# Kernel tuning notes

Measured on AMD Instinct MI355X. Metric: run time of the kernel, lower is better.

## Reference

```python
import jax, jax.numpy as jnp
import numpy as np

N_NODES = 50000
N_EDGES = 800000
IN_CH = 256
OUT_CH = 64
HEADS = 4


def setup_inputs() -> dict:
    key = jax.random.key(0)
    k1, k2, k3, k4, k5 = jax.random.split(key, 5)
    x = jax.random.normal(k1, (N_NODES, IN_CH), dtype=jnp.float32)
    edge_index = jax.random.randint(k2, (2, N_EDGES), 0, N_NODES, dtype=jnp.int64)
    # xavier-ish scaled params
    weight = jax.random.normal(k3, (HEADS, IN_CH, OUT_CH), dtype=jnp.float32) * (2.0 / (IN_CH + OUT_CH)) ** 0.5
    att_src = jax.random.normal(k4, (1, HEADS, OUT_CH), dtype=jnp.float32) * 0.1
    att_dst = jax.random.normal(k5, (1, HEADS, OUT_CH), dtype=jnp.float32) * 0.1
    bias = jnp.zeros((HEADS * OUT_CH,), dtype=jnp.float32)
    return {"x": x, "edge_index": edge_index, "weight": weight,
            "att_src": att_src, "att_dst": att_dst, "bias": bias}


def reference(x, edge_index, weight, att_src, att_dst, bias):
    # GATConv forward (eval mode: dropout is identity), vectorized over heads.
    num_nodes = x.shape[0]
    row, col = edge_index[0], edge_index[1]
    # per-head projection: [N, H, C]
    x_h = jnp.einsum('nf,hfc->nhc', x, weight)
    alpha_src = jnp.sum(x_h * att_src[0], axis=-1)   # [N, H]
    alpha_dst = jnp.sum(x_h * att_dst[0], axis=-1)   # [N, H]
    alpha = alpha_src[row] + alpha_dst[col]          # [E, H]
    alpha = jax.nn.leaky_relu(alpha, negative_slope=0.2)
    # segment softmax over edges grouped by destination row (numerically stable)
    alpha_max = jax.ops.segment_max(alpha, row, num_segments=num_nodes)  # [N, H]
    alpha = jnp.exp(alpha - alpha_max[row])
    alpha_sum = jax.ops.segment_sum(alpha, row, num_segments=num_nodes)  # [N, H]
    alpha = alpha / jnp.clip(alpha_sum[row], 1e-16)
    # message passing: scatter-add alpha-weighted source features
    messages = alpha[:, :, None] * x_h[col]                              # [E, H, C]
    out = jax.ops.segment_sum(messages, row, num_segments=num_nodes)    # [N, H, C]
    out = out.reshape(num_nodes, -1) + bias                              # concat heads
    return out
```

## Files before the change

### kernel.cpp

```cpp
#include <hip/hip_runtime.h>
#include <hip/hip_fp16.h>
#include <math.h>

#define N_IN_CH 256
#define N_OUT   256
#define HEADS   4
#define OUT_CH  64
#define BM      64
#define SCAN_ELEMS 1024

typedef __attribute__((ext_vector_type(8))) short bf16x8;
typedef __attribute__((ext_vector_type(4))) float f32x4;

__device__ __forceinline__ float lrelu(float a) {
  return a >= 0.f ? a : 0.2f * a;
}

__device__ __forceinline__ ushort f2bf(float f) {
  uint u = __float_as_uint(f);
  uint r = (u + 0x7FFFu + ((u >> 16) & 1u)) >> 16;
  return (ushort)r;
}

__device__ __forceinline__ ushort f2h(float f) {
  return __half_as_ushort(__float2half(f));
}
__device__ __forceinline__ float h2f(ushort u) {
  return __half2float(__ushort_as_half(u));
}

__device__ __forceinline__ int wave_scan_partials(const int* __restrict__ partials,
                                                  int nparts, int lane) {
  int pv = (lane < nparts) ? partials[lane] : 0;
  int incl = pv;
#pragma unroll
  for (int d = 1; d < 64; d <<= 1) {
    int t = __shfl_up(incl, d, 64);
    if (lane >= d) incl += t;
  }
  return incl - pv;
}

__global__ void convert_w(const float* __restrict__ w, ushort* __restrict__ bt,
                          int* __restrict__ counts, int nnodes) {
  const int idx = blockIdx.x * 256 + threadIdx.x;
  if (idx < nnodes) counts[idx] = 0;
  const int n = idx >> 8, k = idx & 255;
  const int h = n >> 6, c = n & 63;
  bt[idx] = f2bf(w[h * (N_IN_CH * OUT_CH) + k * OUT_CH + c]);
}

__global__ void count_kernel(const int* __restrict__ row, int* __restrict__ counts,
                             int* __restrict__ rank, int nedges) {
  int e = blockIdx.x * blockDim.x + threadIdx.x;
  if (e < nedges) rank[e] = atomicAdd(&counts[row[e]], 1);
}

__global__ __launch_bounds__(256) void proj_scan(
    const float* __restrict__ x, const ushort* __restrict__ bt,
    const float* __restrict__ att_src, const float* __restrict__ att_dst,
    ushort* __restrict__ xh, float* __restrict__ asrc, float* __restrict__ adst,
    int nnodes, int nblocksA,
    const int* __restrict__ counts, int* __restrict__ offsets,
    int* __restrict__ partials) {
  __shared__ ushort at[BM * N_IN_CH];
  const int tid = threadIdx.x;

  if (blockIdx.x >= nblocksA) {
    __shared__ int wsum[4];
    const int sb = blockIdx.x - nblocksA;
    const int base = sb * SCAN_ELEMS + tid * 4;
    const int n = nnodes;
    int v0 = (base + 0 < n) ? counts[base + 0] : 0;
    int v1 = (base + 1 < n) ? counts[base + 1] : 0;
    int v2 = (base + 2 < n) ? counts[base + 2] : 0;
    int v3 = (base + 3 < n) ? counts[base + 3] : 0;
    const int tsum = v0 + v1 + v2 + v3;
    const int lane = tid & 63;
    const int wid = tid >> 6;
    int incl = tsum;
#pragma unroll
    for (int d = 1; d < 64; d <<= 1) {
      int t = __shfl_up(incl, d, 64);
      if (lane >= d) incl += t;
    }
    if (lane == 63) wsum[wid] = incl;
    __syncthreads();
    int wexcl = incl - tsum;
    int bexcl = 0;
#pragma unroll
    for (int wq = 0; wq < 4; ++wq) bexcl += (wq < wid) ? wsum[wq] : 0;
    const int te = bexcl + wexcl;
    if (base + 0 <= n) offsets[base + 0] = te;
    if (base + 1 <= n) offsets[base + 1] = te + v0;
    if (base + 2 <= n) offsets[base + 2] = te + v0 + v1;
    if (base + 3 <= n) offsets[base + 3] = te + v0 + v1 + v2;
    if (tid == 0) partials[sb] = wsum[0] + wsum[1] + wsum[2] + wsum[3];
    return;
  }

  const int wave = tid >> 6;
  const int lane = tid & 63;
  const int n0 = blockIdx.x * BM;

  {
    const int rsub = tid >> 6;
    const int cf = (tid & 63) * 4;
    const int cb = cf * 2;
#pragma unroll
    for (int it = 0; it < 16; ++it) {
      const int row_ = it * 4 + rsub;
      const int grow = n0 + row_;
      float4 xv = make_float4(0.f, 0.f, 0.f, 0.f);
      if (grow < nnodes) xv = *(const float4*)&x[(size_t)grow * N_IN_CH + cf];
      ushort4 b;
      b.x = f2bf(xv.x); b.y = f2bf(xv.y); b.z = f2bf(xv.z); b.w = f2bf(xv.w);
      const int cbs = cb ^ ((row_ & 7) << 4);
      *(ushort4*)((char*)at + row_ * 512 + cbs) = b;
    }
  }
  __syncthreads();

  f32x4 acc[4][4];
#pragma unroll
  for (int mt = 0; mt < 4; ++mt)
#pragma unroll
    for (int nt = 0; nt < 4; ++nt) acc[mt][nt] = (f32x4){0.f, 0.f, 0.f, 0.f};

  const int lmod = lane & 15;
  const int ldiv = lane >> 4;

  for (int ks = 0; ks < 8; ++ks) {
    bf16x8 a[4], b[4];
#pragma unroll
    for (int mt = 0; mt < 4; ++mt) {
      const int row_ = mt * 16 + lmod;
      const int kb = ks * 64 + ldiv * 16;
      const int cbs = kb ^ ((row_ & 7) << 4);
      a[mt] = *(const bf16x8*)((const char*)at + row_ * 512 + cbs);
    }
#pragma unroll
    for (int nt = 0; nt < 4; ++nt) {
      const int n = wave * 64 + nt * 16 + lmod;
      b[nt] = *(const bf16x8*)&bt[(size_t)n * N_IN_CH + ks * 32 + ldiv * 8];
    }
#pragma unroll
    for (int mt = 0; mt < 4; ++mt)
#pragma unroll
      for (int nt = 0; nt < 4; ++nt)
        acc[mt][nt] = __builtin_amdgcn_mfma_f32_16x16x32_bf16(
            a[mt], b[nt], acc[mt][nt], 0, 0, 0);
  }

  float atts[4], attd[4];
#pragma unroll
  for (int nt = 0; nt < 4; ++nt) {
    const int gcol = wave * 64 + nt * 16 + lmod;
    atts[nt] = att_src[gcol];
    attd[nt] = att_dst[gcol];
  }

#pragma unroll
  for (int mt = 0; mt < 4; ++mt) {
#pragma unroll
    for (int reg = 0; reg < 4; ++reg) {
      const int grow = n0 + mt * 16 + ldiv * 4 + reg;
      const bool ok = grow < nnodes;
      float vs = 0.f, vd = 0.f;
#pragma unroll
      for (int nt = 0; nt < 4; ++nt) {
        const float v = acc[mt][nt][reg];
        if (ok) xh[(size_t)grow * N_OUT + wave * 64 + nt * 16 + lmod] = f2h(v);
        vs = fmaf(v, atts[nt], vs);
        vd = fmaf(v, attd[nt], vd);
      }
#pragma unroll
      for (int d = 1; d < 16; d <<= 1) {
        vs += __shfl_xor(vs, d, 64);
        vd += __shfl_xor(vd, d, 64);
      }
      if (lmod == 0 && ok) {
        asrc[grow * HEADS + wave] = vs;
        adst[grow * HEADS + wave] = vd;
      }
    }
  }
}

__global__ void scatter_kernel(const int* __restrict__ row, const int* __restrict__ col,
                               const int* __restrict__ rank,
                               const int* __restrict__ offsets,
                               const int* __restrict__ partials, int nparts,
                               const float* __restrict__ asrc,
                               const float* __restrict__ adst,
                               uint4* __restrict__ erec, int nedges) {
  const int lane = threadIdx.x & 63;
  const int excl = wave_scan_partials(partials, nparts, lane);
  int e = blockIdx.x * blockDim.x + threadIdx.x;
  if (e < nedges) {
    const int r = row[e];
    const int c = col[e];
    const int pos = offsets[r] + __shfl(excl, r >> 10, 64) + rank[e];
    const float4 s = *(const float4*)&asrc[r * 4];
    const float4 d = *(const float4*)&adst[c * 4];
    uint4 rec;
    rec.x = (uint)c;
    rec.y = (uint)f2h(__expf(lrelu(s.x + d.x))) |
            ((uint)f2h(__expf(lrelu(s.y + d.y))) << 16);
    rec.z = (uint)f2h(__expf(lrelu(s.z + d.z))) |
            ((uint)f2h(__expf(lrelu(s.w + d.w))) << 16);
    rec.w = 0u;
    erec[pos] = rec;
  }
}

__global__ __launch_bounds__(256) void gather_kernel(
    const int* __restrict__ offsets,
    const int* __restrict__ partials, int nparts,
    const uint4* __restrict__ erec,
    const ushort* __restrict__ xh, const float* __restrict__ bias,
    float* __restrict__ out, int nnodes) {
  __shared__ float pbuf[4][64 * 4];
  const int wv = threadIdx.x >> 6;
  const int lane = threadIdx.x & 63;
  const int n = blockIdx.x * 4 + wv;
  if (n >= nnodes) return;
  const int excl = wave_scan_partials(partials, nparts, lane);
  const int off = offsets[n] + __shfl(excl, n >> 10, 64);
  const int end = offsets[n + 1] + __shfl(excl, (n + 1) >> 10, 64);
  const int deg = end - off;
  const int half = lane >> 5;
  const int ch8 = (lane & 31) * 8;
  const int hh = (lane & 31) >> 3;

  float4 s4 = make_float4(0.f, 0.f, 0.f, 0.f);
  float a0 = 0.f, a1 = 0.f, a2 = 0.f, a3 = 0.f;
  float a4 = 0.f, a5 = 0.f, a6 = 0.f, a7 = 0.f;

  for (int b = 0; b < deg; b += 64) {
    const int cnt = min(64, deg - b);
    int cl_l = 0;
    float4 p = make_float4(0.f, 0.f, 0.f, 0.f);
    if (lane < cnt) {
      const uint4 rec = erec[off + b + lane];
      cl_l = (int)rec.x;
      p.x = h2f((ushort)(rec.y & 0xFFFFu));
      p.y = h2f((ushort)(rec.y >> 16));
      p.z = h2f((ushort)(rec.z & 0xFFFFu));
      p.w = h2f((ushort)(rec.z >> 16));
      s4.x += p.x; s4.y += p.y; s4.z += p.z; s4.w += p.w;
    }
    *(float4*)&pbuf[wv][lane * 4] = p;

    for (int j = 0; j < cnt; j += 16) {
      int cq[8];
#pragma unroll
      for (int q = 0; q < 8; ++q) cq[q] = __shfl(cl_l, j + 2 * q + half, 64);
      uint4 xq[8];
#pragma unroll
      for (int q = 0; q < 8; ++q)
        xq[q] = *(const uint4*)&xh[(size_t)cq[q] * N_OUT + ch8];

      float wq[8];
#pragma unroll
      for (int q = 0; q < 8; ++q) wq[q] = pbuf[wv][(j + 2 * q + half) * 4 + hh];

#pragma unroll
      for (int q = 0; q < 8; ++q) {
        a0 = fmaf(wq[q], h2f((ushort)(xq[q].x & 0xFFFFu)), a0);
        a1 = fmaf(wq[q], h2f((ushort)(xq[q].x >> 16)), a1);
        a2 = fmaf(wq[q], h2f((ushort)(xq[q].y & 0xFFFFu)), a2);
        a3 = fmaf(wq[q], h2f((ushort)(xq[q].y >> 16)), a3);
        a4 = fmaf(wq[q], h2f((ushort)(xq[q].z & 0xFFFFu)), a4);
        a5 = fmaf(wq[q], h2f((ushort)(xq[q].z >> 16)), a5);
        a6 = fmaf(wq[q], h2f((ushort)(xq[q].w & 0xFFFFu)), a6);
        a7 = fmaf(wq[q], h2f((ushort)(xq[q].w >> 16)), a7);
      }
    }
  }

  a0 += __shfl_xor(a0, 32, 64);
  a1 += __shfl_xor(a1, 32, 64);
  a2 += __shfl_xor(a2, 32, 64);
  a3 += __shfl_xor(a3, 32, 64);
  a4 += __shfl_xor(a4, 32, 64);
  a5 += __shfl_xor(a5, 32, 64);
  a6 += __shfl_xor(a6, 32, 64);
  a7 += __shfl_xor(a7, 32, 64);

#pragma unroll
  for (int d = 1; d < 64; d <<= 1) {
    s4.x += __shfl_xor(s4.x, d, 64);
    s4.y += __shfl_xor(s4.y, d, 64);
    s4.z += __shfl_xor(s4.z, d, 64);
    s4.w += __shfl_xor(s4.w, d, 64);
  }
  const float sh = (hh == 0) ? s4.x : (hh == 1) ? s4.y : (hh == 2) ? s4.z : s4.w;
  const float invh = 1.f / fmaxf(sh, 1e-16f);

  const int wch = ch8 + half * 4;
  const float4 b4 = *(const float4*)&bias[wch];
  float4 o;
  o.x = fmaf(half ? a4 : a0, invh, b4.x);
  o.y = fmaf(half ? a5 : a1, invh, b4.y);
  o.z = fmaf(half ? a6 : a2, invh, b4.z);
  o.w = fmaf(half ? a7 : a3, invh, b4.w);
  *(float4*)&out[(size_t)n * N_OUT + wch] = o;
}

extern "C" void kernel_launch(void* const* d_in, const int* in_sizes, int n_in,
                              void* d_out, int out_size, void* d_ws, size_t ws_size,
                              hipStream_t stream) {
  const float* x        = (const float*)d_in[0];
  const int*   edge_idx = (const int*)d_in[1];
  const float* weight   = (const float*)d_in[2];
  const float* att_src  = (const float*)d_in[3];
  const float* att_dst  = (const float*)d_in[4];
  const float* bias     = (const float*)d_in[5];
  float* out = (float*)d_out;

  const int nnodes = in_sizes[0] / N_IN_CH;
  const int nedges = in_sizes[1] / 2;
  const int* row = edge_idx;
  const int* col = edge_idx + nedges;

  char* wsb = (char*)d_ws;
  size_t woff = 0;
  auto alloc = [&](size_t bytes) -> char* {
    char* p = wsb + woff;
    woff += (bytes + 255) & ~(size_t)255;
    return p;
  };
  ushort* xh    = (ushort*)alloc((size_t)nnodes * N_OUT * sizeof(ushort));
  ushort* bt    = (ushort*)alloc((size_t)N_OUT * N_IN_CH * sizeof(ushort));
  float* asrc   = (float*)alloc((size_t)nnodes * HEADS * sizeof(float));
  float* adst   = (float*)alloc((size_t)nnodes * HEADS * sizeof(float));
  int* counts   = (int*)alloc((size_t)nnodes * sizeof(int));
  int* offsets  = (int*)alloc((size_t)(nnodes + 1) * sizeof(int));
  int* partials = (int*)alloc(256 * sizeof(int));
  int* rank     = (int*)alloc((size_t)nedges * sizeof(int));
  uint4* erec   = (uint4*)alloc((size_t)nedges * sizeof(uint4));

  convert_w<<<256, 256, 0, stream>>>(weight, bt, counts, nnodes);

  const int eblocks = (nedges + 255) / 256;
  count_kernel<<<eblocks, 256, 0, stream>>>(row, counts, rank, nedges);

  const int nblocksA = (nnodes + BM - 1) / BM;
  const int nscan = (nnodes + 1 + SCAN_ELEMS - 1) / SCAN_ELEMS;
  proj_scan<<<nblocksA + nscan, 256, 0, stream>>>(
      x, bt, att_src, att_dst, xh, asrc, adst, nnodes, nblocksA,
      counts, offsets, partials);

  scatter_kernel<<<eblocks, 256, 0, stream>>>(row, col, rank, offsets,
                                              partials, nscan,
                                              asrc, adst, erec, nedges);

  gather_kernel<<<(nnodes + 3) / 4, 256, 0, stream>>>(offsets, partials, nscan,
                                                      erec, xh, bias, out, nnodes);
}
```

Measured before the change: 165.9 us.

## Split projection tile into two half-tiles and pad atomic counters per cacheline

The projection kernel now stages 32 rows of x at a time in shared memory and loops twice over them. This halves LDS use and the accumulator registers, so more blocks can be resident per CU. Separately, the per-node edge counters are spaced 16 ints apart so each atomic increment lands on its own 64-byte line, reducing same-line atomic contention. The cost is an extra sync per half-tile, a 16x larger counter array, and strided reads of that array in the scan.

```diff
diff --git a/kernel.cpp b/kernel.cpp
--- a/kernel.cpp
+++ b/kernel.cpp
@@ -7,6 +7,8 @@
 #define HEADS   4
 #define OUT_CH  64
 #define BM      64
+#define HM      32
+#define CPAD    16
 #define SCAN_ELEMS 1024
 
 typedef __attribute__((ext_vector_type(8))) short bf16x8;
@@ -44,7 +46,7 @@
 __global__ void convert_w(const float* __restrict__ w, ushort* __restrict__ bt,
                           int* __restrict__ counts, int nnodes) {
   const int idx = blockIdx.x * 256 + threadIdx.x;
-  if (idx < nnodes) counts[idx] = 0;
+  if (idx < nnodes) counts[idx * CPAD] = 0;
   const int n = idx >> 8, k = idx & 255;
   const int h = n >> 6, c = n & 63;
   bt[idx] = f2bf(w[h * (N_IN_CH * OUT_CH) + k * OUT_CH + c]);
@@ -53,7 +55,7 @@
 __global__ void count_kernel(const int* __restrict__ row, int* __restrict__ counts,
                              int* __restrict__ rank, int nedges) {
   int e = blockIdx.x * blockDim.x + threadIdx.x;
-  if (e < nedges) rank[e] = atomicAdd(&counts[row[e]], 1);
+  if (e < nedges) rank[e] = atomicAdd(&counts[row[e] * CPAD], 1);
 }
 
 __global__ __launch_bounds__(256) void proj_scan(
@@ -63,7 +65,7 @@
     int nnodes, int nblocksA,
     const int* __restrict__ counts, int* __restrict__ offsets,
     int* __restrict__ partials) {
-  __shared__ ushort at[BM * N_IN_CH];
+  __shared__ ushort at[HM * N_IN_CH];
   const int tid = threadIdx.x;
 
   if (blockIdx.x >= nblocksA) {
@@ -71,10 +73,10 @@
     const int sb = blockIdx.x - nblocksA;
     const int base = sb * SCAN_ELEMS + tid * 4;
     const int n = nnodes;
-    int v0 = (base + 0 < n) ? counts[base + 0] : 0;
-    int v1 = (base + 1 < n) ? counts[base + 1] : 0;
-    int v2 = (base + 2 < n) ? counts[base + 2] : 0;
-    int v3 = (base + 3 < n) ? counts[base + 3] : 0;
+    int v0 = (base + 0 < n) ? counts[(base + 0) * CPAD] : 0;
+    int v1 = (base + 1 < n) ? counts[(base + 1) * CPAD] : 0;
+    int v2 = (base + 2 < n) ? counts[(base + 2) * CPAD] : 0;
+    int v3 = (base + 3 < n) ? counts[(base + 3) * CPAD] : 0;
     const int tsum = v0 + v1 + v2 + v3;
     const int lane = tid & 63;
     const int wid = tid >> 6;
@@ -101,56 +103,8 @@
 
   const int wave = tid >> 6;
   const int lane = tid & 63;
-  const int n0 = blockIdx.x * BM;
-
-  {
-    const int rsub = tid >> 6;
-    const int cf = (tid & 63) * 4;
-    const int cb = cf * 2;
-#pragma unroll
-    for (int it = 0; it < 16; ++it) {
-      const int row_ = it * 4 + rsub;
-      const int grow = n0 + row_;
-      float4 xv = make_float4(0.f, 0.f, 0.f, 0.f);
-      if (grow < nnodes) xv = *(const float4*)&x[(size_t)grow * N_IN_CH + cf];
-      ushort4 b;
-      b.x = f2bf(xv.x); b.y = f2bf(xv.y); b.z = f2bf(xv.z); b.w = f2bf(xv.w);
-      const int cbs = cb ^ ((row_ & 7) << 4);
-      *(ushort4*)((char*)at + row_ * 512 + cbs) = b;
-    }
-  }
-  __syncthreads();
-
-  f32x4 acc[4][4];
-#pragma unroll
-  for (int mt = 0; mt < 4; ++mt)
-#pragma unroll
-    for (int nt = 0; nt < 4; ++nt) acc[mt][nt] = (f32x4){0.f, 0.f, 0.f, 0.f};
-
   const int lmod = lane & 15;
   const int ldiv = lane >> 4;
-
-  for (int ks = 0; ks < 8; ++ks) {
-    bf16x8 a[4], b[4];
-#pragma unroll
-    for (int mt = 0; mt < 4; ++mt) {
-      const int row_ = mt * 16 + lmod;
-      const int kb = ks * 64 + ldiv * 16;
-      const int cbs = kb ^ ((row_ & 7) << 4);
-      a[mt] = *(const bf16x8*)((const char*)at + row_ * 512 + cbs);
-    }
-#pragma unroll
-    for (int nt = 0; nt < 4; ++nt) {
-      const int n = wave * 64 + nt * 16 + lmod;
-      b[nt] = *(const bf16x8*)&bt[(size_t)n * N_IN_CH + ks * 32 + ldiv * 8];
-    }
-#pragma unroll
-    for (int mt = 0; mt < 4; ++mt)
-#pragma unroll
-      for (int nt = 0; nt < 4; ++nt)
-        acc[mt][nt] = __builtin_amdgcn_mfma_f32_16x16x32_bf16(
-            a[mt], b[nt], acc[mt][nt], 0, 0, 0);
-  }
 
   float atts[4], attd[4];
 #pragma unroll
@@ -160,30 +114,81 @@
     attd[nt] = att_dst[gcol];
   }
 
-#pragma unroll
-  for (int mt = 0; mt < 4; ++mt) {
-#pragma unroll
-    for (int reg = 0; reg < 4; ++reg) {
-      const int grow = n0 + mt * 16 + ldiv * 4 + reg;
-      const bool ok = grow < nnodes;
-      float vs = 0.f, vd = 0.f;
+  for (int h0 = 0; h0 < 2; ++h0) {
+    const int n0 = blockIdx.x * BM + h0 * HM;
+
+    {
+      const int rsub = tid >> 6;
+      const int cf = (tid & 63) * 4;
+      const int cb = cf * 2;
+#pragma unroll
+      for (int it = 0; it < 8; ++it) {
+        const int lr = it * 4 + rsub;
+        const int grow = n0 + lr;
+        float4 xv = make_float4(0.f, 0.f, 0.f, 0.f);
+        if (grow < nnodes) xv = *(const float4*)&x[(size_t)grow * N_IN_CH + cf];
+        ushort4 b;
+        b.x = f2bf(xv.x); b.y = f2bf(xv.y); b.z = f2bf(xv.z); b.w = f2bf(xv.w);
+        const int cbs = cb ^ ((lr & 7) << 4);
+        *(ushort4*)((char*)at + lr * 512 + cbs) = b;
+      }
+    }
+    __syncthreads();
+
+    f32x4 acc[2][4];
+#pragma unroll
+    for (int mt = 0; mt < 2; ++mt)
+#pragma unroll
+      for (int nt = 0; nt < 4; ++nt) acc[mt][nt] = (f32x4){0.f, 0.f, 0.f, 0.f};
+
+    for (int ks = 0; ks < 8; ++ks) {
+      bf16x8 a[2], b[4];
+#pragma unroll
+      for (int mt = 0; mt < 2; ++mt) {
+        const int lr = mt * 16 + lmod;
+        const int kb = ks * 64 + ldiv * 16;
+        const int cbs = kb ^ ((lr & 7) << 4);
+        a[mt] = *(const bf16x8*)((const char*)at + lr * 512 + cbs);
+      }
 #pragma unroll
       for (int nt = 0; nt < 4; ++nt) {
-        const float v = acc[mt][nt][reg];
-        if (ok) xh[(size_t)grow * N_OUT + wave * 64 + nt * 16 + lmod] = f2h(v);
-        vs = fmaf(v, atts[nt], vs);
-        vd = fmaf(v, attd[nt], vd);
-      }
-#pragma unroll
-      for (int d = 1; d < 16; d <<= 1) {
-        vs += __shfl_xor(vs, d, 64);
-        vd += __shfl_xor(vd, d, 64);
-      }
-      if (lmod == 0 && ok) {
-        asrc[grow * HEADS + wave] = vs;
-        adst[grow * HEADS + wave] = vd;
-      }
-    }
+        const int n = wave * 64 + nt * 16 + lmod;
+        b[nt] = *(const bf16x8*)&bt[(size_t)n * N_IN_CH + ks * 32 + ldiv * 8];
+      }
+#pragma unroll
+      for (int mt = 0; mt < 2; ++mt)
+#pragma unroll
+        for (int nt = 0; nt < 4; ++nt)
+          acc[mt][nt] = __builtin_amdgcn_mfma_f32_16x16x32_bf16(
+              a[mt], b[nt], acc[mt][nt], 0, 0, 0);
+    }
+
+#pragma unroll
+    for (int mt = 0; mt < 2; ++mt) {
+#pragma unroll
+      for (int reg = 0; reg < 4; ++reg) {
+        const int grow = n0 + mt * 16 + ldiv * 4 + reg;
+        const bool ok = grow < nnodes;
+        float vs = 0.f, vd = 0.f;
+#pragma unroll
+        for (int nt = 0; nt < 4; ++nt) {
+          const float v = acc[mt][nt][reg];
+          if (ok) xh[(size_t)grow * N_OUT + wave * 64 + nt * 16 + lmod] = f2h(v);
+          vs = fmaf(v, atts[nt], vs);
+          vd = fmaf(v, attd[nt], vd);
+        }
+#pragma unroll
+        for (int d = 1; d < 16; d <<= 1) {
+          vs += __shfl_xor(vs, d, 64);
+          vd += __shfl_xor(vd, d, 64);
+        }
+        if (lmod == 0 && ok) {
+          asrc[grow * HEADS + wave] = vs;
+          adst[grow * HEADS + wave] = vd;
+        }
+      }
+    }
+    __syncthreads();
   }
 }
 
@@ -335,7 +340,7 @@
   ushort* bt    = (ushort*)alloc((size_t)N_OUT * N_IN_CH * sizeof(ushort));
   float* asrc   = (float*)alloc((size_t)nnodes * HEADS * sizeof(float));
   float* adst   = (float*)alloc((size_t)nnodes * HEADS * sizeof(float));
-  int* counts   = (int*)alloc((size_t)nnodes * sizeof(int));
+  int* counts   = (int*)alloc((size_t)nnodes * CPAD * sizeof(int));
   int* offsets  = (int*)alloc((size_t)(nnodes + 1) * sizeof(int));
   int* partials = (int*)alloc(256 * sizeof(int));
   int* rank     = (int*)alloc((size_t)nedges * sizeof(int));
```

Result: no change. 164.8 us (-0.7%).
